# Kernel optimization log

Measured on AMD Instinct MI355X. Metric: run time of the kernel, lower is better.

The kernel has to match this reference:

```python
import jax, jax.numpy as jnp
import numpy as np

N_EMBD = 1024
N_HEAD = 16
HEAD_DIM = N_EMBD // N_HEAD


def setup_inputs() -> dict:
    key = jax.random.key(0)
    ks = jax.random.split(key, 5)
    B, S = 2, 2048
    scale = 0.02
    return {
        "hidden_states": jax.random.normal(ks[0], (B, S, N_EMBD), dtype=jnp.float32),
        "w_attn": jax.random.normal(ks[1], (N_EMBD, 3 * N_EMBD), dtype=jnp.float32) * scale,
        "b_attn": jnp.zeros((3 * N_EMBD,), dtype=jnp.float32),
        "w_proj": jax.random.normal(ks[2], (N_EMBD, N_EMBD), dtype=jnp.float32) * scale,
        "b_proj": jnp.zeros((N_EMBD,), dtype=jnp.float32),
    }


def reference(hidden_states, w_attn, b_attn, w_proj, b_proj):
    B, S, _ = hidden_states.shape
    qkv = hidden_states @ w_attn + b_attn                     # [B,S,3E]
    q, k, v = jnp.split(qkv, 3, axis=-1)                      # each [B,S,E]

    def split_heads(t):  # [B,S,E] -> [B,H,S,D]
        return t.reshape(B, S, N_HEAD, HEAD_DIM).transpose(0, 2, 1, 3)

    q, k, v = split_heads(q), split_heads(k), split_heads(v)

    scores = jnp.einsum("bhqd,bhkd->bhqk", q, k) / np.sqrt(HEAD_DIM).astype(np.float32)
    causal = jnp.tril(jnp.ones((S, S), dtype=bool))
    scores = jnp.where(causal[None, None], scores, jnp.float32(-jnp.inf))
    attn = jax.nn.softmax(scores, axis=-1)                    # [B,H,S,S]
    out = jnp.einsum("bhqk,bhkd->bhqd", attn, v)              # [B,H,S,D]
    out = out.transpose(0, 2, 1, 3).reshape(B, S, N_EMBD)     # merge heads
    out = out @ w_proj + b_proj
    return out
```

## Files before the change

kernel.cpp:

```cpp
#include <hip/hip_runtime.h>
#include <hip/hip_bf16.h>


typedef __attribute__((ext_vector_type(4))) float  float4v;
typedef __attribute__((ext_vector_type(8))) short  short8v;
typedef __attribute__((ext_vector_type(4))) short  short4v;

#define ATT_SCALE 0.18033688011112042f

__device__ __forceinline__ short f2bf(float f) {
  union { float f; unsigned u; } v; v.f = f;
  unsigned r = v.u + 0x7fffu + ((v.u >> 16) & 1u);
  return (short)(r >> 16);
}

__device__ __forceinline__ short4v pack_bf16x4(float a, float b, float c, float d) {
  unsigned x0 = __builtin_bit_cast(unsigned, a) + 0x8000u;
  unsigned x1 = __builtin_bit_cast(unsigned, b) + 0x8000u;
  unsigned x2 = __builtin_bit_cast(unsigned, c) + 0x8000u;
  unsigned x3 = __builtin_bit_cast(unsigned, d) + 0x8000u;
  union { unsigned u[2]; short4v s; } r;
  r.u[0] = __builtin_amdgcn_perm(x1, x0, 0x07060302);
  r.u[1] = __builtin_amdgcn_perm(x3, x2, 0x07060302);
  return r.s;
}

__device__ __forceinline__ void gl_lds16(const void* g, void* l) {
  __builtin_amdgcn_global_load_lds(
      (const __attribute__((address_space(1))) unsigned*)g,
      (__attribute__((address_space(3))) unsigned*)l, 16, 0, 0);
}

__global__ __launch_bounds__(256) void prep_kernel(
    const float* __restrict__ hidden, const float* __restrict__ w_attn,
    const float* __restrict__ w_proj, short* __restrict__ hA,
    short* __restrict__ wqkvT, short* __restrict__ wprojT) {
  __shared__ float tile[32][33];
  const int bx = blockIdx.x, t = threadIdx.x;
  if (bx < 4096) {
    const size_t i = ((size_t)bx * 256 + t) * 4;
    float4v v = *(const float4v*)(hidden + i);
    short4v o;
    #pragma unroll
    for (int k = 0; k < 4; k++) o[k] = f2bf(v[k]);
    *(short4v*)(hA + i) = o;
    return;
  }
  const float* in; short* out; int R, C, cx, cy;
  if (bx < 4096 + 3072) {
    in = w_attn; out = wqkvT; R = 1024; C = 3072;
    cx = (bx - 4096) % 96; cy = (bx - 4096) / 96;
  } else {
    in = w_proj; out = wprojT; R = 1024; C = 1024;
    cx = (bx - 7168) % 32; cy = (bx - 7168) / 32;
  }
  const int tx = t & 31, ty = t >> 5;
  const int c0 = cx * 32, r0 = cy * 32;
  #pragma unroll
  for (int i = 0; i < 4; i++)
    tile[ty + i * 8][tx] = in[(size_t)(r0 + ty + i * 8) * C + c0 + tx];
  __syncthreads();
  #pragma unroll
  for (int i = 0; i < 4; i++) {
    const int cc = ty + i * 8;
    out[(size_t)(c0 + cc) * R + r0 + tx] = f2bf(tile[tx][cc]);
  }
}

__global__ __launch_bounds__(256) void transpose_v(
    const short* __restrict__ qkv, short* __restrict__ vA) {
  __shared__ short T[64][72];
  const int st = blockIdx.x;
  const int bh = blockIdx.y;
  const int b = bh >> 4, h = bh & 15;
  const int t = threadIdx.x;
  const int r = t >> 3, c = (t & 7) * 8;
  const size_t base = (size_t)b * 2048 * 3072 + 2048 + h * 64;
  #pragma unroll
  for (int half = 0; half < 2; half++) {
    const int row = r + half * 32;
    *(short8v*)&T[row][c] =
        *(const short8v*)(qkv + base + (size_t)(st * 64 + row) * 3072 + c);
  }
  __syncthreads();
  const int lane = t & 63, dm = t >> 6;
  const int l16 = lane & 15, quad = lane >> 4;
  #pragma unroll
  for (int kwp = 0; kwp < 2; kwp++) {
    short8v o;
    #pragma unroll
    for (int r2 = 0; r2 < 4; r2++) {
      o[r2]     = T[kwp * 32 + quad * 4 + r2][dm * 16 + l16];
      o[4 + r2] = T[kwp * 32 + 16 + quad * 4 + r2][dm * 16 + l16];
    }
    *(short8v*)(vA + (((size_t)(bh * 32 + st) * 8 + kwp * 4 + dm) * 64 + lane) * 8) = o;
  }
}

template<int RB, int OUT_BF16, int SCALE_Q>
__global__ __launch_bounds__(256) void gemm_bt(
    const short* __restrict__ A, const short* __restrict__ Bt,
    const float* __restrict__ bias, void* __restrict__ Cout,
    int M, int N, int K)
{
  __shared__ short As[RB][32];
  __shared__ short Bs[128][32];
  const int MI = RB / 32;
  const int t    = threadIdx.x;
  const int lane = t & 63;
  const int wave = t >> 6;
  const int wm   = (wave >> 1) * (RB / 2);
  const int wn   = (wave & 1) * 64;
  const int l16  = lane & 15;
  const int quad = lane >> 4;
  const int row0 = blockIdx.y * RB;
  const int col0 = blockIdx.x * 128;

  float4v acc[MI][4] = {};

  const int srow = lane >> 2;
  const int scol = (lane & 3) * 8;

  for (int k0 = 0; k0 < K; k0 += 32) {
    if (RB == 128) {
      #pragma unroll
      for (int h = 0; h < 2; h++)
        gl_lds16(A + (size_t)(row0 + wave * 32 + h * 16 + srow) * K + k0 + scol,
                 &As[(wave * 32 + h * 16 + srow) & (RB - 1)][scol]);
    } else {
      gl_lds16(A + (size_t)(row0 + wave * 16 + srow) * K + k0 + scol,
               &As[(wave * 16 + srow) & (RB - 1)][scol]);
    }
    #pragma unroll
    for (int h = 0; h < 2; h++)
      gl_lds16(Bt + (size_t)(col0 + wave * 32 + h * 16 + srow) * K + k0 + scol,
               &Bs[wave * 32 + h * 16 + srow][scol]);
    __syncthreads();
    short8v af[MI], bf[4];
    #pragma unroll
    for (int i = 0; i < MI; i++)
      af[i] = *(const short8v*)&As[wm + i * 16 + l16][quad * 8];
    #pragma unroll
    for (int j = 0; j < 4; j++)
      bf[j] = *(const short8v*)&Bs[wn + j * 16 + l16][quad * 8];
    #pragma unroll
    for (int i = 0; i < MI; i++)
      #pragma unroll
      for (int j = 0; j < 4; j++)
        acc[i][j] = __builtin_amdgcn_mfma_f32_16x16x32_bf16(af[i], bf[j], acc[i][j], 0, 0, 0);
    __syncthreads();
  }

  #pragma unroll
  for (int j = 0; j < 4; j++) {
    const int col = col0 + wn + j * 16 + l16;
    const float sc = (SCALE_Q && col < 1024) ? ATT_SCALE : 1.0f;
    const float bv = bias[col];
    #pragma unroll
    for (int i = 0; i < MI; i++) {
      #pragma unroll
      for (int r = 0; r < 4; r++) {
        const int row = row0 + wm + i * 16 + quad * 4 + r;
        const float v = (acc[i][j][r] + bv) * sc;
        if (OUT_BF16) ((short*)Cout)[(size_t)row * N + col] = f2bf(v);
        else          ((float*)Cout)[(size_t)row * N + col] = v;
      }
    }
  }
}

__global__ __launch_bounds__(256, 2) void attn_mfma(
    const short* __restrict__ qkv, const short* __restrict__ vA,
    short* __restrict__ out)
{
  __shared__ short KA[2][8 * 512];
  __shared__ short VA[2][8 * 512];

  const int bh = blockIdx.y;
  const int b = bh >> 4, h = bh & 15;
  const int p = blockIdx.x;
  const int t = threadIdx.x;
  const int lane = t & 63, w = t >> 6;
  const int l16 = lane & 15, quad = lane >> 4;

  const size_t base = (size_t)b * 2048 * 3072;
  const int qoff = h * 64, koff = 1024 + h * 64;
  const int qgA = p * 64 + w * 16 + l16;
  const int qgB = (31 - p) * 64 + w * 16 + l16;

  short8v qfA[2], qfB[2];
  #pragma unroll
  for (int ks = 0; ks < 2; ks++) {
    qfA[ks] = *(const short8v*)(qkv + base + (size_t)qgA * 3072 + qoff + ks * 32 + quad * 8);
    qfB[ks] = *(const short8v*)(qkv + base + (size_t)qgB * 3072 + qoff + ks * 32 + quad * 8);
  }

  float4v OA[4] = {}, OB[4] = {};
  float lA = 0.0f, lB = 0.0f;

  const int KTN = 32 - p;
  const int id0 = w * 2;
  const int jm0 = id0 & 3, ks0 = id0 >> 2;
  const int id1 = id0 + 1;
  const int jm1 = id1 & 3, ks1 = id1 >> 2;
  const short* kg0 = qkv + base + (size_t)(jm0 * 16 + l16) * 3072 + koff + ks0 * 32 + quad * 8;
  const short* kg1 = qkv + base + (size_t)(jm1 * 16 + l16) * 3072 + koff + ks1 * 32 + quad * 8;
  const short* vg  = vA + (size_t)(bh * 32) * 4096 + lane * 8;

  gl_lds16(kg0, &KA[0][id0 * 512 + lane * 8]);
  gl_lds16(kg1, &KA[0][id1 * 512 + lane * 8]);
  gl_lds16(vg + id0 * 512, &VA[0][id0 * 512 + lane * 8]);
  gl_lds16(vg + id1 * 512, &VA[0][id1 * 512 + lane * 8]);

  for (int kt = 0; kt < KTN; kt++) {
    const int buf = kt & 1;
    __syncthreads();
    if (kt + 1 < KTN) {
      gl_lds16(kg0 + (size_t)(kt + 1) * 64 * 3072, &KA[buf ^ 1][id0 * 512 + lane * 8]);
      gl_lds16(kg1 + (size_t)(kt + 1) * 64 * 3072, &KA[buf ^ 1][id1 * 512 + lane * 8]);
      gl_lds16(vg + (size_t)(kt + 1) * 4096 + id0 * 512, &VA[buf ^ 1][id0 * 512 + lane * 8]);
      gl_lds16(vg + (size_t)(kt + 1) * 4096 + id1 * 512, &VA[buf ^ 1][id1 * 512 + lane * 8]);
    }

    const bool doA = (kt <= p);
    float4v sA[4] = {}, sB[4] = {};
    #pragma unroll
    for (int ks = 0; ks < 2; ks++)
      #pragma unroll
      for (int jm = 0; jm < 4; jm++) {
        const short8v kf = *(const short8v*)&KA[buf][(ks * 4 + jm) * 512 + lane * 8];
        sB[jm] = __builtin_amdgcn_mfma_f32_16x16x32_bf16(kf, qfB[ks], sB[jm], 0, 0, 0);
        if (doA)
          sA[jm] = __builtin_amdgcn_mfma_f32_16x16x32_bf16(kf, qfA[ks], sA[jm], 0, 0, 0);
      }

    if (kt == KTN - 1) {
      #pragma unroll
      for (int jm = 0; jm < 4; jm++) {
        const int kv = kt * 64 + jm * 16 + quad * 4;
        #pragma unroll
        for (int r = 0; r < 4; r++)
          if (kv + r > qgB) sB[jm][r] = -INFINITY;
      }
    }
    if (doA && kt == p) {
      #pragma unroll
      for (int jm = 0; jm < 4; jm++) {
        const int kv = kt * 64 + jm * 16 + quad * 4;
        #pragma unroll
        for (int r = 0; r < 4; r++)
          if (kv + r > qgA) sA[jm][r] = -INFINITY;
      }
    }

    short4v pkA[4], pkB[4];
    #pragma unroll
    for (int jm = 0; jm < 4; jm++) {
      float p0 = exp2f(sB[jm][0]), p1 = exp2f(sB[jm][1]);
      float p2 = exp2f(sB[jm][2]), p3 = exp2f(sB[jm][3]);
      lB += (p0 + p1) + (p2 + p3);
      pkB[jm] = pack_bf16x4(p0, p1, p2, p3);
    }
    if (doA) {
      #pragma unroll
      for (int jm = 0; jm < 4; jm++) {
        float p0 = exp2f(sA[jm][0]), p1 = exp2f(sA[jm][1]);
        float p2 = exp2f(sA[jm][2]), p3 = exp2f(sA[jm][3]);
        lA += (p0 + p1) + (p2 + p3);
        pkA[jm] = pack_bf16x4(p0, p1, p2, p3);
      }
    }

    #pragma unroll
    for (int id = 0; id < 8; id++) {
      const int kwp = id >> 2, dm = id & 3;
      const short8v vv = *(const short8v*)&VA[buf][id * 512 + lane * 8];
      const short4v v0 = {vv[0], vv[1], vv[2], vv[3]};
      const short4v v1 = {vv[4], vv[5], vv[6], vv[7]};
      OB[dm] = __builtin_amdgcn_mfma_f32_16x16x16bf16_1k(v0, pkB[kwp * 2],     OB[dm], 0, 0, 0);
      OB[dm] = __builtin_amdgcn_mfma_f32_16x16x16bf16_1k(v1, pkB[kwp * 2 + 1], OB[dm], 0, 0, 0);
      if (doA) {
        OA[dm] = __builtin_amdgcn_mfma_f32_16x16x16bf16_1k(v0, pkA[kwp * 2],     OA[dm], 0, 0, 0);
        OA[dm] = __builtin_amdgcn_mfma_f32_16x16x16bf16_1k(v1, pkA[kwp * 2 + 1], OA[dm], 0, 0, 0);
      }
    }
  }

  lA += __shfl_xor(lA, 16); lA += __shfl_xor(lA, 32);
  lB += __shfl_xor(lB, 16); lB += __shfl_xor(lB, 32);
  const float ivA = 1.0f / lA, ivB = 1.0f / lB;
  short* oa = out + (size_t)(b * 2048 + qgA) * 1024 + h * 64;
  short* ob = out + (size_t)(b * 2048 + qgB) * 1024 + h * 64;
  #pragma unroll
  for (int dm = 0; dm < 4; dm++) {
    short4v a4, b4;
    #pragma unroll
    for (int r = 0; r < 4; r++) {
      a4[r] = f2bf(OA[dm][r] * ivA);
      b4[r] = f2bf(OB[dm][r] * ivB);
    }
    *(short4v*)(oa + dm * 16 + quad * 4) = a4;
    *(short4v*)(ob + dm * 16 + quad * 4) = b4;
  }
}

extern "C" void kernel_launch(void* const* d_in, const int* in_sizes, int n_in,
                              void* d_out, int out_size, void* d_ws, size_t ws_size,
                              hipStream_t stream) {
  const float* hidden = (const float*)d_in[0];
  const float* w_attn = (const float*)d_in[1];
  const float* b_attn = (const float*)d_in[2];
  const float* w_proj = (const float*)d_in[3];
  const float* b_proj = (const float*)d_in[4];
  float* outp = (float*)d_out;

  char* ws = (char*)d_ws;
  short* hA     = (short*)(ws);
  short* vAbuf  = (short*)(ws);
  short* wqkvT  = (short*)(ws + 8ull  * 1024 * 1024);
  short* wprojT = (short*)(ws + 14ull * 1024 * 1024);
  short* qkvb   = (short*)(ws + 16ull * 1024 * 1024);
  short* aout   = (short*)(ws + 40ull * 1024 * 1024);

  prep_kernel<<<8192, 256, 0, stream>>>(hidden, w_attn, w_proj, hA, wqkvT, wprojT);
  gemm_bt<128, 1, 1><<<dim3(24, 32), 256, 0, stream>>>(hA, wqkvT, b_attn, qkvb, 4096, 3072, 1024);
  transpose_v<<<dim3(32, 32), 256, 0, stream>>>(qkvb, vAbuf);
  attn_mfma<<<dim3(16, 32), 256, 0, stream>>>(qkvb, vAbuf, aout);
  gemm_bt<64, 0, 0><<<dim3(8, 64), 256, 0, stream>>>(aout, wprojT, b_proj, outp, 4096, 1024, 1024);
}
```

Measured before the change: 211.9 us.

## Split attention KV range across two blocks, fuse V transpose into QKV GEMM

The QKV GEMM epilogue now writes V tiles directly in the MFMA-friendly layout, which removes the separate transpose_v kernel. Attention blocks are doubled: long query rows are split into two KV halves that write unnormalized bf16 partials and row sums. A new merge kernel adds the partials and normalizes them. The extra parallelism and the higher occupancy hint are meant to fill the GPU better, at the cost of an extra launch, scratch traffic through the output buffer, and bf16 rounding of the partial sums.

```diff
diff --git a/kernel.cpp b/kernel.cpp
--- a/kernel.cpp
+++ b/kernel.cpp
@@ -12,6 +12,10 @@
   union { float f; unsigned u; } v; v.f = f;
   unsigned r = v.u + 0x7fffu + ((v.u >> 16) & 1u);
   return (short)(r >> 16);
+}
+__device__ __forceinline__ float bf2f(short s) {
+  union { unsigned u; float f; } v; v.u = ((unsigned)(unsigned short)s) << 16;
+  return v.f;
 }
 
 __device__ __forceinline__ short4v pack_bf16x4(float a, float b, float c, float d) {
@@ -67,41 +71,11 @@
   }
 }
 
-__global__ __launch_bounds__(256) void transpose_v(
-    const short* __restrict__ qkv, short* __restrict__ vA) {
-  __shared__ short T[64][72];
-  const int st = blockIdx.x;
-  const int bh = blockIdx.y;
-  const int b = bh >> 4, h = bh & 15;
-  const int t = threadIdx.x;
-  const int r = t >> 3, c = (t & 7) * 8;
-  const size_t base = (size_t)b * 2048 * 3072 + 2048 + h * 64;
-  #pragma unroll
-  for (int half = 0; half < 2; half++) {
-    const int row = r + half * 32;
-    *(short8v*)&T[row][c] =
-        *(const short8v*)(qkv + base + (size_t)(st * 64 + row) * 3072 + c);
-  }
-  __syncthreads();
-  const int lane = t & 63, dm = t >> 6;
-  const int l16 = lane & 15, quad = lane >> 4;
-  #pragma unroll
-  for (int kwp = 0; kwp < 2; kwp++) {
-    short8v o;
-    #pragma unroll
-    for (int r2 = 0; r2 < 4; r2++) {
-      o[r2]     = T[kwp * 32 + quad * 4 + r2][dm * 16 + l16];
-      o[4 + r2] = T[kwp * 32 + 16 + quad * 4 + r2][dm * 16 + l16];
-    }
-    *(short8v*)(vA + (((size_t)(bh * 32 + st) * 8 + kwp * 4 + dm) * 64 + lane) * 8) = o;
-  }
-}
-
-template<int RB, int OUT_BF16, int SCALE_Q>
+template<int RB, int MODE>
 __global__ __launch_bounds__(256) void gemm_bt(
     const short* __restrict__ A, const short* __restrict__ Bt,
     const float* __restrict__ bias, void* __restrict__ Cout,
-    int M, int N, int K)
+    short* __restrict__ vA, int M, int N, int K)
 {
   __shared__ short As[RB][32];
   __shared__ short Bs[128][32];
@@ -151,10 +125,36 @@
     __syncthreads();
   }
 
+  if (MODE == 2 && col0 >= 2048) {
+    const int b  = row0 >> 11;
+    const int hh = ((col0 - 2048) >> 6) + (wn >> 6);
+    const int kt = ((row0 & 2047) >> 6) + (wm >> 6);
+    short* vbase = vA + ((size_t)((b * 16 + hh) * 32 + kt) * 8) * 512;
+    #pragma unroll
+    for (int j = 0; j < 4; j++) {
+      const float bv = bias[col0 + wn + j * 16 + l16];
+      #pragma unroll
+      for (int kwp = 0; kwp < 2; kwp++) {
+        short8v s8;
+        #pragma unroll
+        for (int kw = 0; kw < 2; kw++) {
+          short4v q4 = pack_bf16x4(acc[kwp * 2 + kw][j][0] + bv,
+                                   acc[kwp * 2 + kw][j][1] + bv,
+                                   acc[kwp * 2 + kw][j][2] + bv,
+                                   acc[kwp * 2 + kw][j][3] + bv);
+          #pragma unroll
+          for (int r = 0; r < 4; r++) s8[kw * 4 + r] = q4[r];
+        }
+        *(short8v*)(vbase + ((size_t)(kwp * 4 + j) * 64 + lane) * 8) = s8;
+      }
+    }
+    return;
+  }
+
   #pragma unroll
   for (int j = 0; j < 4; j++) {
     const int col = col0 + wn + j * 16 + l16;
-    const float sc = (SCALE_Q && col < 1024) ? ATT_SCALE : 1.0f;
+    const float sc = (MODE == 2 && col < 1024) ? ATT_SCALE : 1.0f;
     const float bv = bias[col];
     #pragma unroll
     for (int i = 0; i < MI; i++) {
@@ -162,23 +162,26 @@
       for (int r = 0; r < 4; r++) {
         const int row = row0 + wm + i * 16 + quad * 4 + r;
         const float v = (acc[i][j][r] + bv) * sc;
-        if (OUT_BF16) ((short*)Cout)[(size_t)row * N + col] = f2bf(v);
-        else          ((float*)Cout)[(size_t)row * N + col] = v;
-      }
-    }
-  }
-}
-
-__global__ __launch_bounds__(256, 2) void attn_mfma(
+        if (MODE == 2) ((short*)Cout)[(size_t)row * N + col] = f2bf(v);
+        else           ((float*)Cout)[(size_t)row * N + col] = v;
+      }
+    }
+  }
+}
+
+__global__ __launch_bounds__(256, 4) void attn_mfma(
     const short* __restrict__ qkv, const short* __restrict__ vA,
-    short* __restrict__ out)
+    short* __restrict__ O0, short* __restrict__ O1,
+    float* __restrict__ l0p, float* __restrict__ l1p)
 {
   __shared__ short KA[2][8 * 512];
   __shared__ short VA[2][8 * 512];
 
   const int bh = blockIdx.y;
   const int b = bh >> 4, h = bh & 15;
-  const int p = blockIdx.x;
+  const int x = blockIdx.x;
+  const bool h1 = x >= 16;
+  const int p = h1 ? x - 16 : x;
   const int t = threadIdx.x;
   const int lane = t & 63, w = t >> 6;
   const int l16 = lane & 15, quad = lane >> 4;
@@ -187,6 +190,11 @@
   const int qoff = h * 64, koff = 1024 + h * 64;
   const int qgA = p * 64 + w * 16 + l16;
   const int qgB = (31 - p) * 64 + w * 16 + l16;
+
+  const int a_hi = h1 ? 0 : p + 1;
+  const int b_hi = h1 ? 32 - p : 15 - p;
+  const int kt0  = h1 ? 15 - p : 0;
+  const int ktn  = a_hi > b_hi ? a_hi : b_hi;
 
   short8v qfA[2], qfB[2];
   #pragma unroll
@@ -198,43 +206,42 @@
   float4v OA[4] = {}, OB[4] = {};
   float lA = 0.0f, lB = 0.0f;
 
-  const int KTN = 32 - p;
-  const int id0 = w * 2;
+  const int id0 = w * 2, id1 = id0 + 1;
   const int jm0 = id0 & 3, ks0 = id0 >> 2;
-  const int id1 = id0 + 1;
   const int jm1 = id1 & 3, ks1 = id1 >> 2;
   const short* kg0 = qkv + base + (size_t)(jm0 * 16 + l16) * 3072 + koff + ks0 * 32 + quad * 8;
   const short* kg1 = qkv + base + (size_t)(jm1 * 16 + l16) * 3072 + koff + ks1 * 32 + quad * 8;
   const short* vg  = vA + (size_t)(bh * 32) * 4096 + lane * 8;
 
-  gl_lds16(kg0, &KA[0][id0 * 512 + lane * 8]);
-  gl_lds16(kg1, &KA[0][id1 * 512 + lane * 8]);
-  gl_lds16(vg + id0 * 512, &VA[0][id0 * 512 + lane * 8]);
-  gl_lds16(vg + id1 * 512, &VA[0][id1 * 512 + lane * 8]);
-
-  for (int kt = 0; kt < KTN; kt++) {
-    const int buf = kt & 1;
+  gl_lds16(kg0 + (size_t)kt0 * 64 * 3072, &KA[0][id0 * 512 + lane * 8]);
+  gl_lds16(kg1 + (size_t)kt0 * 64 * 3072, &KA[0][id1 * 512 + lane * 8]);
+  gl_lds16(vg + (size_t)kt0 * 4096 + id0 * 512, &VA[0][id0 * 512 + lane * 8]);
+  gl_lds16(vg + (size_t)kt0 * 4096 + id1 * 512, &VA[0][id1 * 512 + lane * 8]);
+
+  for (int kt = kt0; kt < ktn; kt++) {
+    const int buf = (kt - kt0) & 1;
     __syncthreads();
-    if (kt + 1 < KTN) {
+    if (kt + 1 < ktn) {
       gl_lds16(kg0 + (size_t)(kt + 1) * 64 * 3072, &KA[buf ^ 1][id0 * 512 + lane * 8]);
       gl_lds16(kg1 + (size_t)(kt + 1) * 64 * 3072, &KA[buf ^ 1][id1 * 512 + lane * 8]);
       gl_lds16(vg + (size_t)(kt + 1) * 4096 + id0 * 512, &VA[buf ^ 1][id0 * 512 + lane * 8]);
       gl_lds16(vg + (size_t)(kt + 1) * 4096 + id1 * 512, &VA[buf ^ 1][id1 * 512 + lane * 8]);
     }
 
-    const bool doA = (kt <= p);
+    const bool doA = kt < a_hi;
+    const bool doB = kt < b_hi;
+
     float4v sA[4] = {}, sB[4] = {};
     #pragma unroll
     for (int ks = 0; ks < 2; ks++)
       #pragma unroll
       for (int jm = 0; jm < 4; jm++) {
         const short8v kf = *(const short8v*)&KA[buf][(ks * 4 + jm) * 512 + lane * 8];
-        sB[jm] = __builtin_amdgcn_mfma_f32_16x16x32_bf16(kf, qfB[ks], sB[jm], 0, 0, 0);
-        if (doA)
-          sA[jm] = __builtin_amdgcn_mfma_f32_16x16x32_bf16(kf, qfA[ks], sA[jm], 0, 0, 0);
-      }
-
-    if (kt == KTN - 1) {
+        if (doB) sB[jm] = __builtin_amdgcn_mfma_f32_16x16x32_bf16(kf, qfB[ks], sB[jm], 0, 0, 0);
+        if (doA) sA[jm] = __builtin_amdgcn_mfma_f32_16x16x32_bf16(kf, qfA[ks], sA[jm], 0, 0, 0);
+      }
+
+    if (doB && kt == 31 - p) {
       #pragma unroll
       for (int jm = 0; jm < 4; jm++) {
         const int kv = kt * 64 + jm * 16 + quad * 4;
@@ -243,7 +250,7 @@
           if (kv + r > qgB) sB[jm][r] = -INFINITY;
       }
     }
-    if (doA && kt == p) {
+    if (doA && kt == a_hi - 1) {
       #pragma unroll
       for (int jm = 0; jm < 4; jm++) {
         const int kv = kt * 64 + jm * 16 + quad * 4;
@@ -254,12 +261,14 @@
     }
 
     short4v pkA[4], pkB[4];
-    #pragma unroll
-    for (int jm = 0; jm < 4; jm++) {
-      float p0 = exp2f(sB[jm][0]), p1 = exp2f(sB[jm][1]);
-      float p2 = exp2f(sB[jm][2]), p3 = exp2f(sB[jm][3]);
-      lB += (p0 + p1) + (p2 + p3);
-      pkB[jm] = pack_bf16x4(p0, p1, p2, p3);
+    if (doB) {
+      #pragma unroll
+      for (int jm = 0; jm < 4; jm++) {
+        float p0 = exp2f(sB[jm][0]), p1 = exp2f(sB[jm][1]);
+        float p2 = exp2f(sB[jm][2]), p3 = exp2f(sB[jm][3]);
+        lB += (p0 + p1) + (p2 + p3);
+        pkB[jm] = pack_bf16x4(p0, p1, p2, p3);
+      }
     }
     if (doA) {
       #pragma unroll
@@ -277,8 +286,10 @@
       const short8v vv = *(const short8v*)&VA[buf][id * 512 + lane * 8];
       const short4v v0 = {vv[0], vv[1], vv[2], vv[3]};
       const short4v v1 = {vv[4], vv[5], vv[6], vv[7]};
-      OB[dm] = __builtin_amdgcn_mfma_f32_16x16x16bf16_1k(v0, pkB[kwp * 2],     OB[dm], 0, 0, 0);
-      OB[dm] = __builtin_amdgcn_mfma_f32_16x16x16bf16_1k(v1, pkB[kwp * 2 + 1], OB[dm], 0, 0, 0);
+      if (doB) {
+        OB[dm] = __builtin_amdgcn_mfma_f32_16x16x16bf16_1k(v0, pkB[kwp * 2],     OB[dm], 0, 0, 0);
+        OB[dm] = __builtin_amdgcn_mfma_f32_16x16x16bf16_1k(v1, pkB[kwp * 2 + 1], OB[dm], 0, 0, 0);
+      }
       if (doA) {
         OA[dm] = __builtin_amdgcn_mfma_f32_16x16x16bf16_1k(v0, pkA[kwp * 2],     OA[dm], 0, 0, 0);
         OA[dm] = __builtin_amdgcn_mfma_f32_16x16x16bf16_1k(v1, pkA[kwp * 2 + 1], OA[dm], 0, 0, 0);
@@ -288,20 +299,53 @@
 
   lA += __shfl_xor(lA, 16); lA += __shfl_xor(lA, 32);
   lB += __shfl_xor(lB, 16); lB += __shfl_xor(lB, 32);
-  const float ivA = 1.0f / lA, ivB = 1.0f / lB;
-  short* oa = out + (size_t)(b * 2048 + qgA) * 1024 + h * 64;
-  short* ob = out + (size_t)(b * 2048 + qgB) * 1024 + h * 64;
-  #pragma unroll
-  for (int dm = 0; dm < 4; dm++) {
-    short4v a4, b4;
-    #pragma unroll
-    for (int r = 0; r < 4; r++) {
-      a4[r] = f2bf(OA[dm][r] * ivA);
-      b4[r] = f2bf(OB[dm][r] * ivB);
-    }
-    *(short4v*)(oa + dm * 16 + quad * 4) = a4;
-    *(short4v*)(ob + dm * 16 + quad * 4) = b4;
-  }
+  if (!h1) {
+    short* oa = O0 + (size_t)(b * 2048 + qgA) * 1024 + h * 64;
+    short* ob = O0 + (size_t)(b * 2048 + qgB) * 1024 + h * 64;
+    #pragma unroll
+    for (int dm = 0; dm < 4; dm++) {
+      *(short4v*)(oa + dm * 16 + quad * 4) =
+          pack_bf16x4(OA[dm][0], OA[dm][1], OA[dm][2], OA[dm][3]);
+      *(short4v*)(ob + dm * 16 + quad * 4) =
+          pack_bf16x4(OB[dm][0], OB[dm][1], OB[dm][2], OB[dm][3]);
+    }
+    if (quad == 0) {
+      l0p[(b * 2048 + qgA) * 16 + h] = lA;
+      l0p[(b * 2048 + qgB) * 16 + h] = lB;
+    }
+  } else {
+    short* ob = O1 + (size_t)(b * 1024 + qgB - 1024) * 1024 + h * 64;
+    #pragma unroll
+    for (int dm = 0; dm < 4; dm++)
+      *(short4v*)(ob + dm * 16 + quad * 4) =
+          pack_bf16x4(OB[dm][0], OB[dm][1], OB[dm][2], OB[dm][3]);
+    if (quad == 0) l1p[(b * 2048 + qgB) * 16 + h] = lB;
+  }
+}
+
+__global__ __launch_bounds__(256) void merge_attn(
+    const short* __restrict__ O0, const short* __restrict__ O1,
+    const float* __restrict__ l0p, const float* __restrict__ l1p,
+    short* __restrict__ aout)
+{
+  const int idx = blockIdx.x * 256 + threadIdx.x;
+  const int row = idx >> 7;
+  const int cg  = (idx & 127) * 8;
+  const int h   = cg >> 6;
+  const short8v o0 = *(const short8v*)(O0 + (size_t)row * 1024 + cg);
+  short8v outv;
+  if ((row & 2047) >= 1024) {
+    const int b = row >> 11;
+    const short8v o1 = *(const short8v*)(O1 + (size_t)(b * 1024 + (row & 2047) - 1024) * 1024 + cg);
+    const float inv = 1.0f / (l0p[row * 16 + h] + l1p[row * 16 + h]);
+    #pragma unroll
+    for (int k = 0; k < 8; k++) outv[k] = f2bf((bf2f(o0[k]) + bf2f(o1[k])) * inv);
+  } else {
+    const float inv = 1.0f / l0p[row * 16 + h];
+    #pragma unroll
+    for (int k = 0; k < 8; k++) outv[k] = f2bf(bf2f(o0[k]) * inv);
+  }
+  *(short8v*)(aout + (size_t)row * 1024 + cg) = outv;
 }
 
 extern "C" void kernel_launch(void* const* d_in, const int* in_sizes, int n_in,
@@ -316,15 +360,19 @@
 
   char* ws = (char*)d_ws;
   short* hA     = (short*)(ws);
-  short* vAbuf  = (short*)(ws);
+  float* l0p    = (float*)(ws + 8ull  * 1024 * 1024);
+  float* l1p    = (float*)(ws + 8ull  * 1024 * 1024 + 262144);
   short* wqkvT  = (short*)(ws + 8ull  * 1024 * 1024);
   short* wprojT = (short*)(ws + 14ull * 1024 * 1024);
   short* qkvb   = (short*)(ws + 16ull * 1024 * 1024);
+  short* vAbuf  = (short*)(ws + 40ull * 1024 * 1024);
   short* aout   = (short*)(ws + 40ull * 1024 * 1024);
+  short* O0     = (short*)d_out;
+  short* O1     = (short*)d_out + 4ull * 1024 * 1024;
 
   prep_kernel<<<8192, 256, 0, stream>>>(hidden, w_attn, w_proj, hA, wqkvT, wprojT);
-  gemm_bt<128, 1, 1><<<dim3(24, 32), 256, 0, stream>>>(hA, wqkvT, b_attn, qkvb, 4096, 3072, 1024);
-  transpose_v<<<dim3(32, 32), 256, 0, stream>>>(qkvb, vAbuf);
-  attn_mfma<<<dim3(16, 32), 256, 0, stream>>>(qkvb, vAbuf, aout);
-  gemm_bt<64, 0, 0><<<dim3(8, 64), 256, 0, stream>>>(aout, wprojT, b_proj, outp, 4096, 1024, 1024);
-}
+  gemm_bt<128, 2><<<dim3(24, 32), 256, 0, stream>>>(hA, wqkvT, b_attn, qkvb, vAbuf, 4096, 3072, 1024);
+  attn_mfma<<<dim3(32, 32), 256, 0, stream>>>(qkvb, vAbuf, O0, O1, l0p, l1p);
+  merge_attn<<<2048, 256, 0, stream>>>(O0, O1, l0p, l1p, aout);
+  gemm_bt<64, 0><<<dim3(8, 64), 256, 0, stream>>>(aout, wprojT, b_proj, outp, nullptr, 4096, 1024, 1024);
+}
```

Result: slower. 481.7 us (+127.3%).
